# Optimization experiments

Hardware: AMD Instinct MI355X
Metric: run time of the kernel (lower is better)

Reference implementation:

```python
import jax, jax.numpy as jnp
import numpy as np

TEMPERATURE = 0.02


def setup_inputs() -> dict:
    key = jax.random.key(0)
    k1, k2 = jax.random.split(key)
    B, D_PER, DIM = 4096, 2, 1024
    # scale embeddings so sim/temperature stays in a sane range (like normalized embeddings)
    scale = 1.0 / np.sqrt(DIM)
    query_embeds = jax.random.normal(k1, (B, DIM), dtype=jnp.float32) * scale
    doc_embeds = jax.random.normal(k2, (B * D_PER, DIM), dtype=jnp.float32) * scale
    return {
        "query_embeds": query_embeds,
        "doc_embeds": doc_embeds,
        "num_docs_per_sample": D_PER,
    }


def reference(query_embeds, doc_embeds, num_docs_per_sample):
    # Single-device path of the original: all_doc_embeds == doc_embeds,
    # local_rank == 0, pos_global_idx = i * num_docs_per_sample.
    B = query_embeds.shape[0]
    # [B, total_docs] similarity matrix (one batched GEMM instead of per-sample loop)
    logits = (query_embeds @ doc_embeds.T) / TEMPERATURE
    pos_idx = jnp.arange(B) * num_docs_per_sample  # constant docs-per-sample offsets
    pos_logit = jnp.take_along_axis(logits, pos_idx[:, None], axis=1)[:, 0]
    lse = jax.nn.logsumexp(logits, axis=1)
    loss = jnp.sum(lse - pos_logit) / B
    return loss
```

## Files before the change

### kernel.cpp

```cpp
#include <hip/hip_runtime.h>


#define TEMP_INV 50.0f
#define PRESCALE 16.0f
#define SCALE_BYTE 123

typedef int   i32x4 __attribute__((ext_vector_type(4)));
typedef int   i32x8 __attribute__((ext_vector_type(8)));
typedef float f32x4 __attribute__((ext_vector_type(4)));

__global__ void cvt_kernel(const float* __restrict__ Q, const float* __restrict__ Dm,
                           unsigned int* __restrict__ Q8, unsigned int* __restrict__ D8,
                           float* __restrict__ rowsum, int qSlots, int B, int K) {
    const int gid = blockIdx.x * blockDim.x + threadIdx.x;
    if (gid < B) rowsum[gid] = 0.0f;
    const float* src;
    unsigned int* dst;
    int s;
    if (gid < qSlots) { src = Q;  dst = Q8; s = gid; }
    else              { src = Dm; dst = D8; s = gid - qSlots; }
    {
        const int l0 = s & 63;
        s = (s & ~63) | (((l0 & 3) << 4) | (l0 >> 2));
    }
    const int l   = s & 63;
    const int c   = (s >> 6) & 15;
    const int k0b = (s >> 10) & 7;
    const int R   = s >> 13;
    const int row = R * 128 + (c >> 1) * 16 + (l & 15);
    const int k   = k0b * 128 + (c & 1) * 64 + (l >> 4) * 16;
    const float* p = src + (size_t)row * K + k;
    unsigned int w[4];
#pragma unroll
    for (int d = 0; d < 4; ++d) {
        float4 v = *(const float4*)(p + d * 4);
        int t = __builtin_amdgcn_cvt_pk_fp8_f32(v.x * PRESCALE, v.y * PRESCALE, 0, false);
        t = __builtin_amdgcn_cvt_pk_fp8_f32(v.z * PRESCALE, v.w * PRESCALE, t, true);
        w[d] = (unsigned int)t;
    }
    *(uint4*)(dst + (size_t)s * 4) = make_uint4(w[0], w[1], w[2], w[3]);
}

__global__ __launch_bounds__(256, 2) void gemm_expsum_kernel(
        const unsigned int* __restrict__ Q8, const unsigned int* __restrict__ D8,
        const int* __restrict__ dper,
        float* __restrict__ rowsum, float* __restrict__ pos, int K) {
    __shared__ unsigned int Qs[4096];
    __shared__ unsigned int Ds[4096];

    const int tid   = threadIdx.x;
    const int wave  = tid >> 6;
    const int lane  = tid & 63;
    const int lquad = lane >> 4;
    const int lm    = lane & 15;

    const int f   = blockIdx.x;
    const int xcd = f & 7;
    const int sub = f >> 3;
    const int bx  = (xcd & 1) * 16 + (sub & 15);
    const int by  = (xcd >> 1) * 16 + (sub >> 4);

    const int qbase = bx * 128;
    const int dbase = by * 128;
    const int KB    = K >> 7;

    const int slotofs = ((lquad & 1) * 32 + lm) * 4;
    const int aofs = ((wave >> 1) * 8 + (lquad >> 1)) * 256 + slotofs;
    const int bofs = ((wave & 1) * 8 + (lquad >> 1)) * 256 + slotofs;

    const unsigned int* Qg = Q8 + (size_t)bx * KB * 4096;
    const unsigned int* Dg = D8 + (size_t)by * KB * 4096;

    f32x4 acc[16];
#pragma unroll
    for (int t = 0; t < 16; ++t) acc[t] = (f32x4){0.f, 0.f, 0.f, 0.f};

    for (int kb = 0; kb < KB; ++kb) {
#pragma unroll
        for (int q = 0; q < 4; ++q) {
            const int c = wave * 4 + q;
            const unsigned int* g1 = Qg + kb * 4096 + c * 256 + lane * 4;
            __builtin_amdgcn_global_load_lds(
                (const __attribute__((address_space(1))) void*)g1,
                (__attribute__((address_space(3))) void*)(Qs + c * 256 + lane * 4),
                16, 0, 0);
            const unsigned int* g2 = Dg + kb * 4096 + c * 256 + lane * 4;
            __builtin_amdgcn_global_load_lds(
                (const __attribute__((address_space(1))) void*)g2,
                (__attribute__((address_space(3))) void*)(Ds + c * 256 + lane * 4),
                16, 0, 0);
        }
        __syncthreads();

        i32x8 a8[4], b8[4];
#pragma unroll
        for (int i = 0; i < 4; ++i) {
            i32x4 lo = *(const i32x4*)(Qs + aofs + i * 512);
            i32x4 hi = *(const i32x4*)(Qs + aofs + i * 512 + 64);
            a8[i] = __builtin_shufflevector(lo, hi, 0, 1, 2, 3, 4, 5, 6, 7);
        }
#pragma unroll
        for (int j = 0; j < 4; ++j) {
            i32x4 lo = *(const i32x4*)(Ds + bofs + j * 512);
            i32x4 hi = *(const i32x4*)(Ds + bofs + j * 512 + 64);
            b8[j] = __builtin_shufflevector(lo, hi, 0, 1, 2, 3, 4, 5, 6, 7);
        }
#pragma unroll
        for (int i = 0; i < 4; ++i)
#pragma unroll
            for (int j = 0; j < 4; ++j)
                acc[i * 4 + j] = __builtin_amdgcn_mfma_scale_f32_16x16x128_f8f6f4(
                    a8[i], b8[j], acc[i * 4 + j], 0, 0, 0, SCALE_BYTE, 0, SCALE_BYTE);
        __syncthreads();
    }

    const int dp = dper[0];
#pragma unroll
    for (int i = 0; i < 4; ++i)
#pragma unroll
        for (int r = 0; r < 4; ++r) {
            const int gr   = qbase + (wave >> 1) * 64 + 16 * i + 4 * lquad + r;
            const int pcol = gr * dp - dbase;
            float e = 0.0f;
#pragma unroll
            for (int j = 0; j < 4; ++j) {
                float v = acc[i * 4 + j][r];
                if ((wave & 1) * 64 + 16 * j + lm == pcol) pos[gr] = v * TEMP_INV;
                e += __expf(v * TEMP_INV);
            }
            e += __shfl_xor(e, 1);
            e += __shfl_xor(e, 2);
            e += __shfl_xor(e, 4);
            e += __shfl_xor(e, 8);
            if (lm == 0) atomicAdd(&rowsum[gr], e);
        }
}

__global__ void final_kernel(const float* __restrict__ rowsum,
                             const float* __restrict__ pos,
                             float* __restrict__ out, int B) {
    __shared__ float red[16];
    int tid = threadIdx.x;
    float s = 0.0f;
    for (int i = tid; i < B; i += blockDim.x)
        s += __logf(rowsum[i]) - pos[i];
    s += __shfl_xor(s, 32);
    s += __shfl_xor(s, 16);
    s += __shfl_xor(s, 8);
    s += __shfl_xor(s, 4);
    s += __shfl_xor(s, 2);
    s += __shfl_xor(s, 1);
    int w = tid >> 6, l = tid & 63;
    if (l == 0) red[w] = s;
    __syncthreads();
    if (tid == 0) {
        float t = 0.0f;
        int nw = blockDim.x >> 6;
        for (int i = 0; i < nw; ++i) t += red[i];
        out[0] = t / (float)B;
    }
}

extern "C" void kernel_launch(void* const* d_in, const int* in_sizes, int n_in,
                              void* d_out, int out_size, void* d_ws, size_t ws_size,
                              hipStream_t stream) {
    const float* Q   = (const float*)d_in[0];
    const float* Dm  = (const float*)d_in[1];
    const int* dper  = (const int*)d_in[2];
    float* out = (float*)d_out;

    const int DIM  = 1024;
    const int B    = in_sizes[0] / DIM;
    const int Ntot = in_sizes[1] / DIM;

    unsigned int* Q8 = (unsigned int*)d_ws;
    unsigned int* D8 = Q8 + (size_t)B * DIM / 4;
    float* rowsum = (float*)(D8 + (size_t)Ntot * DIM / 4);
    float* pos = rowsum + B;

    const int qSlots = B * DIM / 16;
    const int dSlots = Ntot * DIM / 16;
    cvt_kernel<<<(qSlots + dSlots) / 256, 256, 0, stream>>>(
        Q, Dm, Q8, D8, rowsum, qSlots, B, DIM);

    const int nblk = (B / 128) * (Ntot / 128);
    gemm_expsum_kernel<<<nblk, 256, 0, stream>>>(Q8, D8, dper, rowsum, pos, DIM);

    final_kernel<<<1, 1024, 0, stream>>>(rowsum, pos, out, B);
}
```

Before: 128.7 us.

## Use 256x256 tiles with 8 waves and double-buffered LDS prefetch in FP8 GEMM

```diff
diff --git a/kernel.cpp b/kernel.cpp
--- a/kernel.cpp
+++ b/kernel.cpp
@@ -41,92 +41,121 @@
     *(uint4*)(dst + (size_t)s * 4) = make_uint4(w[0], w[1], w[2], w[3]);
 }
 
-__global__ __launch_bounds__(256, 2) void gemm_expsum_kernel(
+__global__ __launch_bounds__(512, 2) void gemm_expsum_kernel(
         const unsigned int* __restrict__ Q8, const unsigned int* __restrict__ D8,
         const int* __restrict__ dper,
         float* __restrict__ rowsum, float* __restrict__ pos, int K) {
-    __shared__ unsigned int Qs[4096];
-    __shared__ unsigned int Ds[4096];
+    __shared__ unsigned int BUF[32768];
 
     const int tid   = threadIdx.x;
     const int wave  = tid >> 6;
     const int lane  = tid & 63;
+    const int wr    = wave >> 2;
+    const int wc    = wave & 3;
     const int lquad = lane >> 4;
     const int lm    = lane & 15;
+    const int lh2   = lquad >> 1;
 
     const int f   = blockIdx.x;
     const int xcd = f & 7;
     const int sub = f >> 3;
-    const int bx  = (xcd & 1) * 16 + (sub & 15);
-    const int by  = (xcd >> 1) * 16 + (sub >> 4);
-
-    const int qbase = bx * 128;
-    const int dbase = by * 128;
-    const int KB    = K >> 7;
+    const int bx  = (xcd & 1) * 8 + (sub & 7);
+    const int by  = (xcd >> 1) * 8 + (sub >> 3);
+
+    const int KB = K >> 7;
+
+    const unsigned int* sbase = (wave < 4) ? Q8 : D8;
+    const int bb = (wave < 4) ? bx : by;
+    unsigned int sidx[8];
+    unsigned int dofs[8];
+#pragma unroll
+    for (int q = 0; q < 8; ++q) {
+        const int fl = (wave & 3) * 8 + q;
+        const int rb = fl >> 4;
+        const int c  = fl & 15;
+        sidx[q] = (unsigned int)((2 * bb + rb) * (KB * 4096) + c * 256 + lane * 4);
+        dofs[q] = (unsigned int)((wave * 8 + q) * 256 + lane * 4);
+    }
 
     const int slotofs = ((lquad & 1) * 32 + lm) * 4;
-    const int aofs = ((wave >> 1) * 8 + (lquad >> 1)) * 256 + slotofs;
-    const int bofs = ((wave & 1) * 8 + (lquad >> 1)) * 256 + slotofs;
-
-    const unsigned int* Qg = Q8 + (size_t)bx * KB * 4096;
-    const unsigned int* Dg = D8 + (size_t)by * KB * 4096;
-
-    f32x4 acc[16];
-#pragma unroll
-    for (int t = 0; t < 16; ++t) acc[t] = (f32x4){0.f, 0.f, 0.f, 0.f};
-
-    for (int kb = 0; kb < KB; ++kb) {
-#pragma unroll
-        for (int q = 0; q < 4; ++q) {
-            const int c = wave * 4 + q;
-            const unsigned int* g1 = Qg + kb * 4096 + c * 256 + lane * 4;
-            __builtin_amdgcn_global_load_lds(
-                (const __attribute__((address_space(1))) void*)g1,
-                (__attribute__((address_space(3))) void*)(Qs + c * 256 + lane * 4),
-                16, 0, 0);
-            const unsigned int* g2 = Dg + kb * 4096 + c * 256 + lane * 4;
-            __builtin_amdgcn_global_load_lds(
-                (const __attribute__((address_space(1))) void*)g2,
-                (__attribute__((address_space(3))) void*)(Ds + c * 256 + lane * 4),
-                16, 0, 0);
+    const int ao0 = (wr * 16 + lh2) * 256 + slotofs;
+    const int bo0 = 8192 + (wc * 8 + lh2) * 256 + slotofs;
+
+    f32x4 acc[32];
+#pragma unroll
+    for (int t = 0; t < 32; ++t) acc[t] = (f32x4){0.f, 0.f, 0.f, 0.f};
+
+#pragma unroll
+    for (int q = 0; q < 8; ++q)
+        __builtin_amdgcn_global_load_lds(
+            (const __attribute__((address_space(1))) void*)(sbase + sidx[q]),
+            (__attribute__((address_space(3))) void*)(BUF + dofs[q]), 16, 0, 0);
+    asm volatile("s_waitcnt vmcnt(0)" ::: "memory");
+    __builtin_amdgcn_s_barrier();
+
+    int cur = 0;
+    for (int kb = 0; kb < KB; ++kb, cur ^= 1) {
+        const bool pf = (kb + 1 < KB);
+        const unsigned int* bp = BUF + cur * 16384;
+        unsigned int* np = BUF + (cur ^ 1) * 16384;
+        const unsigned int soff = (unsigned int)((kb + 1) * 4096);
+#pragma unroll
+        for (int p = 0; p < 4; ++p) {
+            const int Mh = p >> 1, Nh = p & 1;
+            i32x8 a8[4], b8[2];
+#pragma unroll
+            for (int i = 0; i < 4; ++i) {
+                const int off = ao0 + (Mh * 4 + i) * 512;
+                i32x4 lo = *(const i32x4*)(bp + off);
+                i32x4 hi = *(const i32x4*)(bp + off + 64);
+                a8[i] = __builtin_shufflevector(lo, hi, 0, 1, 2, 3, 4, 5, 6, 7);
+            }
+#pragma unroll
+            for (int j = 0; j < 2; ++j) {
+                const int off = bo0 + (Nh * 2 + j) * 512;
+                i32x4 lo = *(const i32x4*)(bp + off);
+                i32x4 hi = *(const i32x4*)(bp + off + 64);
+                b8[j] = __builtin_shufflevector(lo, hi, 0, 1, 2, 3, 4, 5, 6, 7);
+            }
+            if (pf) {
+#pragma unroll
+                for (int q = 0; q < 2; ++q)
+                    __builtin_amdgcn_global_load_lds(
+                        (const __attribute__((address_space(1))) void*)(sbase + sidx[p * 2 + q] + soff),
+                        (__attribute__((address_space(3))) void*)(np + dofs[p * 2 + q]), 16, 0, 0);
+            }
+            __builtin_amdgcn_s_barrier();
+            asm volatile("s_waitcnt lgkmcnt(0)" ::: "memory");
+            __builtin_amdgcn_s_setprio(1);
+#pragma unroll
+            for (int i = 0; i < 4; ++i)
+#pragma unroll
+                for (int j = 0; j < 2; ++j)
+                    acc[(Mh * 4 + i) * 4 + (Nh * 2 + j)] =
+                        __builtin_amdgcn_mfma_scale_f32_16x16x128_f8f6f4(
+                            a8[i], b8[j], acc[(Mh * 4 + i) * 4 + (Nh * 2 + j)],
+                            0, 0, 0, SCALE_BYTE, 0, SCALE_BYTE);
+            __builtin_amdgcn_s_setprio(0);
+            if (p == 3 && pf)
+                asm volatile("s_waitcnt vmcnt(0)" ::: "memory");
+            __builtin_amdgcn_s_barrier();
         }
-        __syncthreads();
-
-        i32x8 a8[4], b8[4];
-#pragma unroll
-        for (int i = 0; i < 4; ++i) {
-            i32x4 lo = *(const i32x4*)(Qs + aofs + i * 512);
-            i32x4 hi = *(const i32x4*)(Qs + aofs + i * 512 + 64);
-            a8[i] = __builtin_shufflevector(lo, hi, 0, 1, 2, 3, 4, 5, 6, 7);
-        }
-#pragma unroll
-        for (int j = 0; j < 4; ++j) {
-            i32x4 lo = *(const i32x4*)(Ds + bofs + j * 512);
-            i32x4 hi = *(const i32x4*)(Ds + bofs + j * 512 + 64);
-            b8[j] = __builtin_shufflevector(lo, hi, 0, 1, 2, 3, 4, 5, 6, 7);
-        }
-#pragma unroll
-        for (int i = 0; i < 4; ++i)
-#pragma unroll
-            for (int j = 0; j < 4; ++j)
-                acc[i * 4 + j] = __builtin_amdgcn_mfma_scale_f32_16x16x128_f8f6f4(
-                    a8[i], b8[j], acc[i * 4 + j], 0, 0, 0, SCALE_BYTE, 0, SCALE_BYTE);
-        __syncthreads();
-    }
-
-    const int dp = dper[0];
-#pragma unroll
-    for (int i = 0; i < 4; ++i)
+    }
+
+    const int dp  = dper[0];
+    const int gr0 = bx * 256 + wr * 128 + 4 * lquad;
+    const int gc0 = by * 256 + wc * 64 + lm;
+#pragma unroll
+    for (int i = 0; i < 8; ++i)
 #pragma unroll
         for (int r = 0; r < 4; ++r) {
-            const int gr   = qbase + (wave >> 1) * 64 + 16 * i + 4 * lquad + r;
-            const int pcol = gr * dp - dbase;
+            const int gr = gr0 + 16 * i + r;
             float e = 0.0f;
 #pragma unroll
             for (int j = 0; j < 4; ++j) {
-                float v = acc[i * 4 + j][r];
-                if ((wave & 1) * 64 + 16 * j + lm == pcol) pos[gr] = v * TEMP_INV;
-                e += __expf(v * TEMP_INV);
+                float v = acc[i * 4 + j][r] * TEMP_INV;
+                if (gr * dp == gc0 + 16 * j) pos[gr] = v;
+                e += __expf(v);
             }
             e += __shfl_xor(e, 1);
             e += __shfl_xor(e, 2);
@@ -183,8 +212,8 @@
     cvt_kernel<<<(qSlots + dSlots) / 256, 256, 0, stream>>>(
         Q, Dm, Q8, D8, rowsum, qSlots, B, DIM);
 
-    const int nblk = (B / 128) * (Ntot / 128);
-    gemm_expsum_kernel<<<nblk, 256, 0, stream>>>(Q8, D8, dper, rowsum, pos, DIM);
+    const int nblk = (B / 256) * (Ntot / 256);
+    gemm_expsum_kernel<<<nblk, 512, 0, stream>>>(Q8, D8, dper, rowsum, pos, DIM);
 
     final_kernel<<<1, 1024, 0, stream>>>(rowsum, pos, out, B);
 }
```

Result: slower. 339.9 us (+164.0%).
